# Optimization experiments

Measured on AMD Instinct MI355X. Metric: run time of the kernel, lower is better.

Reference implementation:

```python
import jax, jax.numpy as jnp
import numpy as np

K = 11            # kernel size
D = K * K         # flow input size = 121
HID = 15          # MADE hidden size
NB = 5            # n_blocks
ALPHA = 1e-6      # post_process inverse-logit alpha
EPS = 1e-5        # BatchNorm eps
SCALE = 2         # 1/scale_factor
LOG2PI = float(np.log(2.0 * np.pi))


def _degrees(block):
    # MAF flips input ordering between successive MADE blocks
    d = jnp.arange(D)
    return d if block % 2 == 0 else d[::-1]


def _masks(deg_in):
    # MADE masks: hidden degrees = arange(HID) % (D-1)
    dh = jnp.arange(HID) % (D - 1)
    m1 = (dh[:, None] >= deg_in[None, :]).astype(jnp.float32)   # [HID, D]
    m2 = (deg_in[:, None] > dh[None, :]).astype(jnp.float32)    # [D, HID] (strict for output)
    m2 = jnp.concatenate([m2, m2], axis=0)                      # [2D, HID] (m and loga share mask)
    return m1, m2


def _made_inverse(u, W1, b1, W2, b2, deg):
    m1, m2 = _masks(deg)
    Wm1 = (W1 * m1).T   # [D, HID]
    Wm2 = (W2 * m2).T   # [HID, 2D]

    def net(x):
        h = jax.nn.relu(x @ Wm1 + b1)
        out = h @ Wm2 + b2
        return out[:, :D], out[:, D:]

    def step(x, i):
        m, loga = net(x)
        x = x.at[:, i].set(u[:, i] * jnp.exp(loga[:, i]) + m[:, i])
        return x, None

    x, _ = jax.lax.scan(step, jnp.zeros_like(u), deg)
    # so evaluating on fully-filled x equals the torch loop's last-iteration loga
    _, loga = net(x)
    return x, loga


def _flow_inverse(u, W1, b1, W2, b2, bn_log_gamma, bn_beta, bn_mean, bn_var):
    # FlowSequential.inverse: iterate blocks in reverse, each block = [MADE, BatchNorm]
    x = u
    sum_ldj = jnp.zeros_like(u)
    for b in reversed(range(NB)):
        # BatchNorm inverse (eval mode, running stats)
        var, mean = bn_var[b], bn_mean[b]
        lg, beta = bn_log_gamma[b], bn_beta[b]
        x = (x - beta) * jnp.exp(-lg) * jnp.sqrt(var + EPS) + mean
        sum_ldj = sum_ldj + (0.5 * jnp.log(var + EPS) - lg)[None, :]
        # MADE inverse
        x, loga = _made_inverse(x, W1[b], b1[b], W2[b], b2[b], _degrees(b))
        sum_ldj = sum_ldj + loga
    return x, sum_ldj


def _post_process(x):
    x = (jax.nn.sigmoid(x) - ALPHA) / (1.0 - 2.0 * ALPHA)
    x = x / jnp.sum(x, axis=1, keepdims=True)   # kernel sums to 1
    return x.reshape(x.shape[0], 1, K, K)


def setup_inputs() -> dict:
    key = jax.random.key(0)
    ks = jax.random.split(key, 10)
    s = 0.1
    return {
        "input_tensor": jax.random.normal(ks[0], (1, 3, 4096, 4096), jnp.float32),
        "kernel_code": jax.random.normal(ks[1], (1, D), jnp.float32),
        "W1": jax.random.normal(ks[2], (NB, HID, D), jnp.float32) * s,
        "b1": jax.random.normal(ks[3], (NB, HID), jnp.float32) * s,
        "W2": jax.random.normal(ks[4], (NB, 2 * D, HID), jnp.float32) * s,
        "b2": jax.random.normal(ks[5], (NB, 2 * D), jnp.float32) * s,
        "bn_log_gamma": jax.random.normal(ks[6], (NB, D), jnp.float32) * s,
        "bn_beta": jax.random.normal(ks[7], (NB, D), jnp.float32) * s,
        "bn_mean": jax.random.normal(ks[8], (NB, D), jnp.float32) * s,
        "bn_var": jax.random.uniform(ks[9], (NB, D), jnp.float32) * 0.5 + 0.5,
    }


def reference(input_tensor, kernel_code, W1, b1, W2, b2, bn_log_gamma, bn_beta, bn_mean, bn_var):
    # kp.inverse: flow inverse + log prob under base dist
    x, sum_ldj = _flow_inverse(kernel_code, W1, b1, W2, b2, bn_log_gamma, bn_beta, bn_mean, bn_var)
    base_lp = jnp.sum(-0.5 * kernel_code**2 - 0.5 * LOG2PI, axis=1)
    logprob = base_lp - jnp.sum(sum_ldj, axis=1)   # (unused downstream, kept for fidelity)
    out_k = _post_process(x)                        # [1,1,K,K]
    # grouped conv + stride-2 subsample: conv-with-stride == full conv then [0::2] slice
    w = jnp.broadcast_to(out_k, (3, 1, K, K))
    out_put = jax.lax.conv_general_dilated(
        input_tensor, w, window_strides=(SCALE, SCALE), padding='VALID',
        dimension_numbers=('NCHW', 'OIHW', 'NCHW'), feature_group_count=3)
    return out_put, out_k[0, 0]
```

## Files before the change

kernel.cpp:

```cpp
#include <hip/hip_runtime.h>

#define DD   121
#define NHID 15
#define NBLK 5
#define KS   11
#define IW   4096
#define OW   2043

#define ROR_ADD(v, N)                                                         \
  v += __int_as_float(__builtin_amdgcn_update_dpp(                            \
      0, __float_as_int(v), 0x120 + (N), 0xF, 0xF, true))

__device__ __forceinline__ void stage_weights(
    float* W1d, float* W2d, float* b2d, float* b1d,
    const float* __restrict__ W1, const float* __restrict__ W2,
    const float* __restrict__ b2, const float* __restrict__ b1,
    int blk, int t0, int nt)
{
    const float* W1b = W1 + blk * NHID * DD;
    const float* W2b = W2 + blk * 2 * DD * NHID;
    const float* b2b = b2 + blk * 2 * DD;
    for (int i = t0; i < NHID * DD; i += nt) W1d[i] = W1b[i];
    for (int k = t0; k < DD * NHID; k += nt) {
        const int idx = k / NHID, j = k - idx * NHID;
        W2d[idx*32 + 2*j]     = W2b[idx*NHID + j];
        W2d[idx*32 + 2*j + 1] = W2b[(DD + idx)*NHID + j];
    }
    for (int i = t0; i < DD; i += nt) {
        W2d[i*32 + 30] = 0.f;
        W2d[i*32 + 31] = 0.f;
        b2d[2*i]     = b2b[i];
        b2d[2*i + 1] = b2b[DD + i];
    }
    for (int i = t0; i < NHID; i += nt) b1d[i] = b1[blk*NHID + i];
}

__global__ __launch_bounds__(128) void flow_kernel(
    const float* __restrict__ kc,
    const float* __restrict__ W1, const float* __restrict__ b1,
    const float* __restrict__ W2, const float* __restrict__ b2,
    const float* __restrict__ lg, const float* __restrict__ beta,
    const float* __restrict__ mean, const float* __restrict__ var,
    float* __restrict__ kout)
{
    __shared__ float xs[DD];
    __shared__ float us[DD];
    __shared__ float W1s[2][NHID * DD];
    __shared__ float W2p[2][DD * 32];
    __shared__ float b2p[2][DD * 2];
    __shared__ float b1s[2][16];

    const int tid  = threadIdx.x;
    const int wv   = tid >> 6;
    const int lane = tid & 63;

    stage_weights(W1s[0], W2p[0], b2p[0], b1s[0], W1, W2, b2, b1, NBLK - 1, tid, 128);
    if (tid < DD) xs[tid] = kc[tid];
    __syncthreads();

    for (int b = NBLK - 1; b >= 0; --b) {
        const int buf = (NBLK - 1 - b) & 1;
        if (wv == 1) {
            if (b > 0)
                stage_weights(W1s[buf^1], W2p[buf^1], b2p[buf^1], b1s[buf^1],
                              W1, W2, b2, b1, b - 1, lane, 64);
        } else {
            for (int i = lane; i < DD; i += 64) {
                float s = sqrtf(var[b*DD + i] + 1e-5f);
                us[i] = (xs[i] - beta[b*DD + i]) * __expf(-lg[b*DD + i]) * s + mean[b*DD + i];
            }
            const int evenb = ((b & 1) == 0);
            if (lane < 16) {
                const int j  = lane;
                const int jc = (j < NHID) ? j : (NHID - 1);
                float pre_h = (j < NHID) ? b1s[buf][j] : 0.f;

                auto step = [&](int t, int iS, float2 wpS, float w1S, float uvS, float2 bpS) {
                    float h  = (j < t && j < NHID) ? fmaxf(pre_h, 0.f) : 0.f;
                    float pm = h * wpS.x;
                    float pa = h * wpS.y;
                    ROR_ADD(pm, 1); ROR_ADD(pa, 1);
                    ROR_ADD(pm, 2); ROR_ADD(pa, 2);
                    ROR_ADD(pm, 4); ROR_ADD(pa, 4);
                    ROR_ADD(pm, 8); ROR_ADD(pa, 8);
                    const float xv = fmaf(uvS, __expf(pa + bpS.y), pm + bpS.x);
                    if (j >= t && j < NHID) pre_h = fmaf(xv, w1S, pre_h);
                    if (j == 0) xs[iS] = xv;
                };

                int iA, iB, iC, iD;
                float2 wpA, wpB, wpC, wpD, bpA, bpB, bpC, bpD;
                float  w1A, w1B, w1C, w1D, uvA, uvB, uvC, uvD;

                #define PRELOAD(S, T) { const int tt = (T);                                 \
                    i##S  = evenb ? tt : (DD - 1 - tt);                                     \
                    wp##S = *(const float2*)&W2p[buf][i##S*32 + 2*j];                       \
                    w1##S = W1s[buf][jc*DD + i##S];                                         \
                    uv##S = us[i##S];                                                       \
                    bp##S = *(const float2*)&b2p[buf][2*i##S]; }

                #define QSTEP(S, TCUR, TNEXT) {                                             \
                    int tt = (TNEXT); if (tt > DD - 1) tt = DD - 1;                         \
                    const int ip = evenb ? tt : (DD - 1 - tt);                              \
                    const float2 wpN = *(const float2*)&W2p[buf][ip*32 + 2*j];              \
                    const float  w1N = W1s[buf][jc*DD + ip];                                \
                    const float  uvN = us[ip];                                              \
                    const float2 bpN = *(const float2*)&b2p[buf][2*ip];                     \
                    step((TCUR), i##S, wp##S, w1##S, uv##S, bp##S);                         \
                    i##S = ip; wp##S = wpN; w1##S = w1N; uv##S = uvN; bp##S = bpN; }

                PRELOAD(A, 0) PRELOAD(B, 1) PRELOAD(C, 2) PRELOAD(D, 3)
                #pragma unroll 1
                for (int it = 0; it < 30; ++it) {
                    QSTEP(A, 4*it + 0, 4*it + 4)
                    QSTEP(B, 4*it + 1, 4*it + 5)
                    QSTEP(C, 4*it + 2, 4*it + 6)
                    QSTEP(D, 4*it + 3, 4*it + 7)
                }
                step(DD - 1, iA, wpA, w1A, uvA, bpA);
                #undef PRELOAD
                #undef QSTEP
            }
        }
        __syncthreads();
    }

    if (tid < 64) {
        const float A = 1e-6f;
        float y0, y1 = 0.f;
        {
            float v = xs[tid];
            y0 = (1.f / (1.f + __expf(-v)) - A) / (1.f - 2.f*A);
        }
        if (tid + 64 < DD) {
            float v = xs[tid + 64];
            y1 = (1.f / (1.f + __expf(-v)) - A) / (1.f - 2.f*A);
        }
        float s = y0 + y1;
        #pragma unroll
        for (int off = 32; off >= 1; off >>= 1) s += __shfl_xor(s, off, 64);
        kout[tid] = y0 / s;
        if (tid + 64 < DD) kout[tid + 64] = y1 / s;
    }
}

#define TIY 41
#define SE  80

__global__ __launch_bounds__(256) void conv_kernel(
    const float* __restrict__ in, const float* __restrict__ kf,
    float* __restrict__ out)
{
    __shared__ __align__(16) float E[TIY * SE];
    __shared__ __align__(16) float O[TIY * SE];

    const int tid = threadIdx.x;
    const int cch = blockIdx.z;
    const int ox0 = blockIdx.x * 64;
    const int oy0 = blockIdx.y * 16;
    const int gx0 = ox0 * 2;
    const int gy0 = oy0 * 2;

    const float* __restrict__ inc = in + (size_t)cch * IW * IW;
    {
        const int l  = tid & 31;
        const int c4 = l * 4;
        for (int r = tid >> 5; r < TIY; r += 8) {
            const int gy = gy0 + r;
            const float* rowp = inc + (size_t)gy * IW + gx0;
            float4 g = make_float4(0.f, 0.f, 0.f, 0.f);
            if (gy < IW) g = *(const float4*)(rowp + c4);
            *(float2*)&E[r*SE + (c4 >> 1)] = make_float2(g.x, g.z);
            *(float2*)&O[r*SE + (c4 >> 1)] = make_float2(g.y, g.w);
            if (l < 9) {
                const int ct = 128 + l;
                float v = 0.f;
                if (gy < IW && (gx0 + ct) < IW) v = rowp[ct];
                if (ct & 1) O[r*SE + (ct >> 1)] = v;
                else        E[r*SE + (ct >> 1)] = v;
            }
        }
    }
    __syncthreads();

    const int tx = tid & 15;
    const int ty = tid >> 4;

    float acc[4] = {0.f, 0.f, 0.f, 0.f};

    #pragma unroll
    for (int ky = 0; ky < 11; ++ky) {
        const int row = 2*ty + ky;
        const float4 ea = *(const float4*)&E[row*SE + 4*tx];
        const float4 eb = *(const float4*)&E[row*SE + 4*tx + 4];
        const float  ec =                  E[row*SE + 4*tx + 8];
        const float4 oa = *(const float4*)&O[row*SE + 4*tx];
        const float4 ob = *(const float4*)&O[row*SE + 4*tx + 4];
        const float ev[9] = {ea.x,ea.y,ea.z,ea.w,eb.x,eb.y,eb.z,eb.w,ec};
        const float ov[8] = {oa.x,oa.y,oa.z,oa.w,ob.x,ob.y,ob.z,ob.w};
        #pragma unroll
        for (int m = 0; m < 6; ++m) {
            const float we = kf[ky*KS + 2*m];
            #pragma unroll
            for (int j = 0; j < 4; ++j)
                acc[j] = fmaf(ev[m + j], we, acc[j]);
        }
        #pragma unroll
        for (int m = 0; m < 5; ++m) {
            const float wo = kf[ky*KS + 2*m + 1];
            #pragma unroll
            for (int j = 0; j < 4; ++j)
                acc[j] = fmaf(ov[m + j], wo, acc[j]);
        }
    }

    const int oy = oy0 + ty;
    if (oy < OW) {
        const size_t base = ((size_t)cch * OW + oy) * OW;
        if ((ox0 + 63) < OW) {
            #pragma unroll
            for (int j = 0; j < 4; ++j)
                out[base + ox0 + 4*tx + j] = acc[j];
        } else {
            #pragma unroll
            for (int j = 0; j < 4; ++j) {
                const int ox = ox0 + 4*tx + j;
                if (ox < OW) out[base + ox] = acc[j];
            }
        }
    }
}

extern "C" void kernel_launch(void* const* d_in, const int* in_sizes, int n_in,
                              void* d_out, int out_size, void* d_ws, size_t ws_size,
                              hipStream_t stream)
{
    const float* in   = (const float*)d_in[0];
    const float* kc   = (const float*)d_in[1];
    const float* W1   = (const float*)d_in[2];
    const float* b1   = (const float*)d_in[3];
    const float* W2   = (const float*)d_in[4];
    const float* b2   = (const float*)d_in[5];
    const float* lg   = (const float*)d_in[6];
    const float* beta = (const float*)d_in[7];
    const float* mean = (const float*)d_in[8];
    const float* var  = (const float*)d_in[9];

    float* out  = (float*)d_out;
    float* kout = out + (size_t)3 * OW * OW;

    flow_kernel<<<dim3(1), dim3(128), 0, stream>>>(kc, W1, b1, W2, b2, lg, beta, mean, var, kout);

    dim3 grid((OW + 63) / 64, (OW + 15) / 16, 3);
    conv_kernel<<<grid, dim3(256), 0, stream>>>(in, kout, out);
}
```

Baseline: 232.0 us.

## Stream row pairs through single-wave conv blocks with rotating accumulators

The conv kernel becomes a 64-thread block that walks down a 13-output-row strip, 256 outputs wide. It loads two input rows per step into registers, prefetching the next pair while the current pair is computed, and stages them into small even/odd LDS buffers. Each row pair feeds a ring of six output-row accumulators, so every input row is read once per strip and no large 2D tile is held in shared memory. The aim is to overlap global loads with FMA work and drop the block-wide barrier. The cost is relying on wave-level ordering of LDS accesses with no explicit sync, plus higher register pressure from 24 accumulators.

```diff
diff --git a/kernel.cpp b/kernel.cpp
--- a/kernel.cpp
+++ b/kernel.cpp
@@ -144,89 +144,155 @@
     }
 }
 
-#define TIY 41
-#define SE  80
-
-__global__ __launch_bounds__(256) void conv_kernel(
+#define HSTRIP 13
+#define NPAIRG 3
+
+__global__ __launch_bounds__(64) void conv_kernel(
     const float* __restrict__ in, const float* __restrict__ kf,
     float* __restrict__ out)
 {
-    __shared__ __align__(16) float E[TIY * SE];
-    __shared__ __align__(16) float O[TIY * SE];
-
-    const int tid = threadIdx.x;
-    const int cch = blockIdx.z;
-    const int ox0 = blockIdx.x * 64;
-    const int oy0 = blockIdx.y * 16;
+    __shared__ __align__(16) float Ee[2][264];
+    __shared__ __align__(16) float Oo[2][264];
+
+    const int l   = threadIdx.x;
+    const int ox0 = blockIdx.x * 256;
     const int gx0 = ox0 * 2;
+    const int oy0 = blockIdx.y * HSTRIP;
     const int gy0 = oy0 * 2;
-
-    const float* __restrict__ inc = in + (size_t)cch * IW * IW;
-    {
-        const int l  = tid & 31;
-        const int c4 = l * 4;
-        for (int r = tid >> 5; r < TIY; r += 8) {
-            const int gy = gy0 + r;
-            const float* rowp = inc + (size_t)gy * IW + gx0;
-            float4 g = make_float4(0.f, 0.f, 0.f, 0.f);
-            if (gy < IW) g = *(const float4*)(rowp + c4);
-            *(float2*)&E[r*SE + (c4 >> 1)] = make_float2(g.x, g.z);
-            *(float2*)&O[r*SE + (c4 >> 1)] = make_float2(g.y, g.w);
-            if (l < 9) {
-                const int ct = 128 + l;
-                float v = 0.f;
-                if (gy < IW && (gx0 + ct) < IW) v = rowp[ct];
-                if (ct & 1) O[r*SE + (ct >> 1)] = v;
-                else        E[r*SE + (ct >> 1)] = v;
-            }
-        }
-    }
-    __syncthreads();
-
-    const int tx = tid & 15;
-    const int ty = tid >> 4;
-
-    float acc[4] = {0.f, 0.f, 0.f, 0.f};
-
-    #pragma unroll
-    for (int ky = 0; ky < 11; ++ky) {
-        const int row = 2*ty + ky;
-        const float4 ea = *(const float4*)&E[row*SE + 4*tx];
-        const float4 eb = *(const float4*)&E[row*SE + 4*tx + 4];
-        const float  ec =                  E[row*SE + 4*tx + 8];
-        const float4 oa = *(const float4*)&O[row*SE + 4*tx];
-        const float4 ob = *(const float4*)&O[row*SE + 4*tx + 4];
-        const float ev[9] = {ea.x,ea.y,ea.z,ea.w,eb.x,eb.y,eb.z,eb.w,ec};
-        const float ov[8] = {oa.x,oa.y,oa.z,oa.w,ob.x,ob.y,ob.z,ob.w};
+    const int ch  = blockIdx.z;
+
+    const float* __restrict__ inc  = in  + (size_t)ch * IW * IW;
+    float*       __restrict__ outc = out + (size_t)ch * OW * OW;
+    const int xlim = IW - gx0;
+
+    float acc[6][4] = {};
+
+    float4 g0a, g0b, g1a, g1b;
+    float  g0t, g1t;
+
+    auto gload = [&](int p) {
+        const int ir0 = gy0 + 2*p;
+        const float* r0 = inc + (size_t)ir0 * IW + gx0;
+        const float* r1 = r0 + IW;
+        const bool ok0 = (ir0     < IW);
+        const bool ok1 = (ir0 + 1 < IW);
+        g0a = make_float4(0.f,0.f,0.f,0.f); g0b = g0a; g1a = g0a; g1b = g0a;
+        g0t = 0.f; g1t = 0.f;
+        if (ok0) { g0a = *(const float4*)(r0 + 4*l); g0b = *(const float4*)(r0 + 256 + 4*l); }
+        if (ok1) { g1a = *(const float4*)(r1 + 4*l); g1b = *(const float4*)(r1 + 256 + 4*l); }
+        if (l < 9 && 512 + l < xlim) {
+            if (ok0) g0t = r0[512 + l];
+            if (ok1) g1t = r1[512 + l];
+        }
+    };
+
+    auto lwrite = [&]() {
+        *(float2*)&Ee[0][2*l]       = make_float2(g0a.x, g0a.z);
+        *(float2*)&Oo[0][2*l]       = make_float2(g0a.y, g0a.w);
+        *(float2*)&Ee[0][128 + 2*l] = make_float2(g0b.x, g0b.z);
+        *(float2*)&Oo[0][128 + 2*l] = make_float2(g0b.y, g0b.w);
+        *(float2*)&Ee[1][2*l]       = make_float2(g1a.x, g1a.z);
+        *(float2*)&Oo[1][2*l]       = make_float2(g1a.y, g1a.w);
+        *(float2*)&Ee[1][128 + 2*l] = make_float2(g1b.x, g1b.z);
+        *(float2*)&Oo[1][128 + 2*l] = make_float2(g1b.y, g1b.w);
+        if (l < 9) {
+            const int i = 256 + (l >> 1);
+            if ((l & 1) == 0) { Ee[0][i] = g0t; Ee[1][i] = g1t; }
+            else              { Oo[0][i] = g0t; Oo[1][i] = g1t; }
+        }
+    };
+
+    gload(0);
+    lwrite();
+
+    #pragma unroll 1
+    for (int g = 0; g < NPAIRG; ++g) {
         #pragma unroll
-        for (int m = 0; m < 6; ++m) {
-            const float we = kf[ky*KS + 2*m];
+        for (int u = 0; u < 6; ++u) {
+            const int p = 6*g + u;
+
+            float ev0[9], ov0[8], ev1[9], ov1[8];
+            {
+                const float4 a = *(const float4*)&Ee[0][4*l];
+                const float4 b = *(const float4*)&Ee[0][4*l + 4];
+                const float  t =                  Ee[0][4*l + 8];
+                const float4 c = *(const float4*)&Oo[0][4*l];
+                const float4 d = *(const float4*)&Oo[0][4*l + 4];
+                ev0[0]=a.x; ev0[1]=a.y; ev0[2]=a.z; ev0[3]=a.w;
+                ev0[4]=b.x; ev0[5]=b.y; ev0[6]=b.z; ev0[7]=b.w; ev0[8]=t;
+                ov0[0]=c.x; ov0[1]=c.y; ov0[2]=c.z; ov0[3]=c.w;
+                ov0[4]=d.x; ov0[5]=d.y; ov0[6]=d.z; ov0[7]=d.w;
+            }
+            {
+                const float4 a = *(const float4*)&Ee[1][4*l];
+                const float4 b = *(const float4*)&Ee[1][4*l + 4];
+                const float  t =                  Ee[1][4*l + 8];
+                const float4 c = *(const float4*)&Oo[1][4*l];
+                const float4 d = *(const float4*)&Oo[1][4*l + 4];
+                ev1[0]=a.x; ev1[1]=a.y; ev1[2]=a.z; ev1[3]=a.w; ev1[4]=b.x;
+                ev1[5]=b.y; ev1[6]=b.z; ev1[7]=b.w; ev1[8]=t;
+                ov1[0]=c.x; ov1[1]=c.y; ov1[2]=c.z; ov1[3]=c.w;
+                ov1[4]=d.x; ov1[5]=d.y; ov1[6]=d.z; ov1[7]=d.w;
+            }
+
+            gload(p + 1);
+
             #pragma unroll
-            for (int j = 0; j < 4; ++j)
-                acc[j] = fmaf(ev[m + j], we, acc[j]);
-        }
-        #pragma unroll
-        for (int m = 0; m < 5; ++m) {
-            const float wo = kf[ky*KS + 2*m + 1];
+            for (int a = 0; a < 6; ++a) {
+                const int s  = (u + 5 - a) % 6;
+                const int ky = 2*a;
+                #pragma unroll
+                for (int m = 0; m < 6; ++m) {
+                    const float w = kf[ky*KS + 2*m];
+                    #pragma unroll
+                    for (int j = 0; j < 4; ++j)
+                        acc[s][j] = fmaf(ev0[m + j], w, acc[s][j]);
+                }
+                #pragma unroll
+                for (int m = 0; m < 5; ++m) {
+                    const float w = kf[ky*KS + 2*m + 1];
+                    #pragma unroll
+                    for (int j = 0; j < 4; ++j)
+                        acc[s][j] = fmaf(ov0[m + j], w, acc[s][j]);
+                }
+            }
             #pragma unroll
-            for (int j = 0; j < 4; ++j)
-                acc[j] = fmaf(ov[m + j], wo, acc[j]);
-        }
-    }
-
-    const int oy = oy0 + ty;
-    if (oy < OW) {
-        const size_t base = ((size_t)cch * OW + oy) * OW;
-        if ((ox0 + 63) < OW) {
-            #pragma unroll
-            for (int j = 0; j < 4; ++j)
-                out[base + ox0 + 4*tx + j] = acc[j];
-        } else {
-            #pragma unroll
-            for (int j = 0; j < 4; ++j) {
-                const int ox = ox0 + 4*tx + j;
-                if (ox < OW) out[base + ox] = acc[j];
-            }
+            for (int a = 0; a < 5; ++a) {
+                const int s  = (u + 5 - a) % 6;
+                const int ky = 2*a + 1;
+                #pragma unroll
+                for (int m = 0; m < 6; ++m) {
+                    const float w = kf[ky*KS + 2*m];
+                    #pragma unroll
+                    for (int j = 0; j < 4; ++j)
+                        acc[s][j] = fmaf(ev1[m + j], w, acc[s][j]);
+                }
+                #pragma unroll
+                for (int m = 0; m < 5; ++m) {
+                    const float w = kf[ky*KS + 2*m + 1];
+                    #pragma unroll
+                    for (int j = 0; j < 4; ++j)
+                        acc[s][j] = fmaf(ov1[m + j], w, acc[s][j]);
+                }
+            }
+
+            if (p >= 5) {
+                const int oy = oy0 + p - 5;
+                if (oy < OW) {
+                    float* op = outc + (size_t)oy * OW + ox0 + 4*l;
+                    if (ox0 + 4*l + 3 < OW) {
+                        op[0] = acc[u][0]; op[1] = acc[u][1];
+                        op[2] = acc[u][2]; op[3] = acc[u][3];
+                    } else {
+                        #pragma unroll
+                        for (int j = 0; j < 4; ++j)
+                            if (ox0 + 4*l + j < OW) op[j] = acc[u][j];
+                    }
+                }
+            }
+            acc[u][0] = acc[u][1] = acc[u][2] = acc[u][3] = 0.f;
+
+            lwrite();
         }
     }
 }
@@ -251,6 +317,6 @@
 
     flow_kernel<<<dim3(1), dim3(128), 0, stream>>>(kc, W1, b1, W2, b2, lg, beta, mean, var, kout);
 
-    dim3 grid((OW + 63) / 64, (OW + 15) / 16, 3);
-    conv_kernel<<<grid, dim3(256), 0, stream>>>(in, kout, out);
+    dim3 grid(8, (OW + HSTRIP - 1) / HSTRIP, 3);
+    conv_kernel<<<grid, dim3(64), 0, stream>>>(in, kout, out);
 }
```

New measurement: 303.2 us. +30.7%, slower.

## Rewrite conv as register-tiled full-row blocks without shared memory, XCD-aware ordering

Applied to the files above, without the earlier changes.

The strided 11x11 convolution is restructured so each block computes two full output rows for one channel. Each thread loads 28 contiguous input floats per input row straight from global memory into registers and accumulates 8 outputs for both rows, dropping the LDS staging and barrier. Block indices are remapped so consecutive row pairs land on the same XCD, aiming for L2 reuse of the overlapping input rows. Each thread now reads input rows directly with no shared-memory sharing between neighbouring threads, which raises redundant global/L1 traffic and register pressure.

```diff
diff --git a/kernel.cpp b/kernel.cpp
--- a/kernel.cpp
+++ b/kernel.cpp
@@ -144,90 +144,90 @@
     }
 }
 
-#define TIY 41
-#define SE  80
-
 __global__ __launch_bounds__(256) void conv_kernel(
     const float* __restrict__ in, const float* __restrict__ kf,
     float* __restrict__ out)
 {
-    __shared__ __align__(16) float E[TIY * SE];
-    __shared__ __align__(16) float O[TIY * SE];
-
-    const int tid = threadIdx.x;
-    const int cch = blockIdx.z;
-    const int ox0 = blockIdx.x * 64;
-    const int oy0 = blockIdx.y * 16;
-    const int gx0 = ox0 * 2;
-    const int gy0 = oy0 * 2;
-
-    const float* __restrict__ inc = in + (size_t)cch * IW * IW;
+    const int tx = threadIdx.x;
+    int py = blockIdx.x;
     {
-        const int l  = tid & 31;
-        const int c4 = l * 4;
-        for (int r = tid >> 5; r < TIY; r += 8) {
-            const int gy = gy0 + r;
-            const float* rowp = inc + (size_t)gy * IW + gx0;
-            float4 g = make_float4(0.f, 0.f, 0.f, 0.f);
-            if (gy < IW) g = *(const float4*)(rowp + c4);
-            *(float2*)&E[r*SE + (c4 >> 1)] = make_float2(g.x, g.z);
-            *(float2*)&O[r*SE + (c4 >> 1)] = make_float2(g.y, g.w);
-            if (l < 9) {
-                const int ct = 128 + l;
-                float v = 0.f;
-                if (gy < IW && (gx0 + ct) < IW) v = rowp[ct];
-                if (ct & 1) O[r*SE + (ct >> 1)] = v;
-                else        E[r*SE + (ct >> 1)] = v;
-            }
-        }
-    }
-    __syncthreads();
-
-    const int tx = tid & 15;
-    const int ty = tid >> 4;
-
-    float acc[4] = {0.f, 0.f, 0.f, 0.f};
-
-    #pragma unroll
-    for (int ky = 0; ky < 11; ++ky) {
-        const int row = 2*ty + ky;
-        const float4 ea = *(const float4*)&E[row*SE + 4*tx];
-        const float4 eb = *(const float4*)&E[row*SE + 4*tx + 4];
-        const float  ec =                  E[row*SE + 4*tx + 8];
-        const float4 oa = *(const float4*)&O[row*SE + 4*tx];
-        const float4 ob = *(const float4*)&O[row*SE + 4*tx + 4];
-        const float ev[9] = {ea.x,ea.y,ea.z,ea.w,eb.x,eb.y,eb.z,eb.w,ec};
-        const float ov[8] = {oa.x,oa.y,oa.z,oa.w,ob.x,ob.y,ob.z,ob.w};
+        const int N = (OW + 1) / 2;
+        const int q = N / 8, r = N % 8;
+        const int xcd = py & 7, idx = py >> 3;
+        py = (xcd < r) ? xcd * (q + 1) + idx
+                       : r * (q + 1) + (xcd - r) * q + idx;
+    }
+    const int ch  = blockIdx.y;
+    const int oy0 = 2 * py;
+    const int gy0 = 4 * py;
+
+    const float* __restrict__ inc  = in  + (size_t)ch * IW * IW;
+    float*       __restrict__ outc = out + (size_t)ch * OW * OW;
+    const int wbase = 16 * tx;
+
+    float acc0[8] = {0.f,0.f,0.f,0.f,0.f,0.f,0.f,0.f};
+    float acc1[8] = {0.f,0.f,0.f,0.f,0.f,0.f,0.f,0.f};
+
+    #pragma unroll 1
+    for (int iy = 0; iy < 13; ++iy) {
+        const int gy = gy0 + iy;
+        if (gy >= IW) break;
+        const float* rp = inc + (size_t)gy * IW + wbase;
+
+        float4 w0, w1, w2, w3, w4, w5, w6;
+        if (tx < 255) {
+            w0 = *(const float4*)(rp);      w1 = *(const float4*)(rp + 4);
+            w2 = *(const float4*)(rp + 8);  w3 = *(const float4*)(rp + 12);
+            w4 = *(const float4*)(rp + 16); w5 = *(const float4*)(rp + 20);
+            w6 = *(const float4*)(rp + 24);
+        } else {
+            w0 = *(const float4*)(rp);      w1 = *(const float4*)(rp + 4);
+            w2 = *(const float4*)(rp + 8);  w3 = *(const float4*)(rp + 12);
+            w4 = make_float4(0.f,0.f,0.f,0.f); w5 = w4; w6 = w4;
+        }
+        float wv[28];
+        wv[0]=w0.x;  wv[1]=w0.y;  wv[2]=w0.z;  wv[3]=w0.w;
+        wv[4]=w1.x;  wv[5]=w1.y;  wv[6]=w1.z;  wv[7]=w1.w;
+        wv[8]=w2.x;  wv[9]=w2.y;  wv[10]=w2.z; wv[11]=w2.w;
+        wv[12]=w3.x; wv[13]=w3.y; wv[14]=w3.z; wv[15]=w3.w;
+        wv[16]=w4.x; wv[17]=w4.y; wv[18]=w4.z; wv[19]=w4.w;
+        wv[20]=w5.x; wv[21]=w5.y; wv[22]=w5.z; wv[23]=w5.w;
+        wv[24]=w6.x; wv[25]=w6.y; wv[26]=w6.z; wv[27]=w6.w;
+
+        if (iy <= 10) {
+            const float* kr = kf + iy * KS;
+            #pragma unroll
+            for (int kx = 0; kx < 11; ++kx) {
+                const float kw = kr[kx];
+                #pragma unroll
+                for (int j = 0; j < 8; ++j)
+                    acc0[j] = fmaf(wv[2*j + kx], kw, acc0[j]);
+            }
+        }
+        if (iy >= 2) {
+            const float* kr = kf + (iy - 2) * KS;
+            #pragma unroll
+            for (int kx = 0; kx < 11; ++kx) {
+                const float kw = kr[kx];
+                #pragma unroll
+                for (int j = 0; j < 8; ++j)
+                    acc1[j] = fmaf(wv[2*j + kx], kw, acc1[j]);
+            }
+        }
+    }
+
+    const int ox0 = 8 * tx;
+    {
+        float* op = outc + (size_t)oy0 * OW + ox0;
         #pragma unroll
-        for (int m = 0; m < 6; ++m) {
-            const float we = kf[ky*KS + 2*m];
-            #pragma unroll
-            for (int j = 0; j < 4; ++j)
-                acc[j] = fmaf(ev[m + j], we, acc[j]);
-        }
+        for (int j = 0; j < 8; ++j)
+            if (ox0 + j < OW) op[j] = acc0[j];
+    }
+    if (oy0 + 1 < OW) {
+        float* op = outc + (size_t)(oy0 + 1) * OW + ox0;
         #pragma unroll
-        for (int m = 0; m < 5; ++m) {
-            const float wo = kf[ky*KS + 2*m + 1];
-            #pragma unroll
-            for (int j = 0; j < 4; ++j)
-                acc[j] = fmaf(ov[m + j], wo, acc[j]);
-        }
-    }
-
-    const int oy = oy0 + ty;
-    if (oy < OW) {
-        const size_t base = ((size_t)cch * OW + oy) * OW;
-        if ((ox0 + 63) < OW) {
-            #pragma unroll
-            for (int j = 0; j < 4; ++j)
-                out[base + ox0 + 4*tx + j] = acc[j];
-        } else {
-            #pragma unroll
-            for (int j = 0; j < 4; ++j) {
-                const int ox = ox0 + 4*tx + j;
-                if (ox < OW) out[base + ox] = acc[j];
-            }
-        }
+        for (int j = 0; j < 8; ++j)
+            if (ox0 + j < OW) op[j] = acc1[j];
     }
 }
 
@@ -251,6 +251,6 @@
 
     flow_kernel<<<dim3(1), dim3(128), 0, stream>>>(kc, W1, b1, W2, b2, lg, beta, mean, var, kout);
 
-    dim3 grid((OW + 63) / 64, (OW + 15) / 16, 3);
+    dim3 grid((OW + 1) / 2, 3);
     conv_kernel<<<grid, dim3(256), 0, stream>>>(in, kout, out);
 }
```

New measurement: 209.9 us. -9.5%, faster.
